# Performance work log

Measured on AMD Instinct MI355X. Metric: run time of the kernel, lower is better.

The kernel has to match this reference:

```python
import jax, jax.numpy as jnp
import numpy as np

N_NODES = 50000
N_EDGES = 320000
B = 4096          # subgraph batch: users/items/subg nodes
IN_N = 64         # in_nfeats
IN_E = 16         # in_efeats
OUT_E = 2 * IN_E  # out_edge_feats = in_efeats*2
H = 4             # num_heads
D = 64            # latent dim per layer (latent_dim=[64,64])
L = 2             # num EGAT layers


def setup_inputs() -> dict:
    key = jax.random.key(0)
    ks = iter(jax.random.split(key, 48))
    def nrm(shape, s=0.05):
        return jax.random.normal(next(ks), shape, dtype=jnp.float32) * s
    inp = {}
    inp['x'] = jax.random.normal(next(ks), (N_NODES, IN_N), dtype=jnp.float32)
    inp['efeat'] = jax.random.normal(next(ks), (N_EDGES, IN_E), dtype=jnp.float32)
    inp['efeat2'] = jax.random.normal(next(ks), (N_EDGES, IN_N), dtype=jnp.float32)
    inp['edge_mask'] = (jax.random.uniform(next(ks), (N_EDGES,)) > 0.1).astype(jnp.float32)
    inp['edge_mask2'] = (jax.random.uniform(next(ks), (N_EDGES,)) > 0.1).astype(jnp.float32)
    inp['src'] = jax.random.randint(next(ks), (N_EDGES,), 0, N_NODES, dtype=jnp.int32)
    inp['dst'] = jax.random.randint(next(ks), (N_EDGES,), 0, N_NODES, dtype=jnp.int32)
    inp['user_idx'] = jnp.arange(0, B, dtype=jnp.int32)          # ntype==0
    inp['item_idx'] = jnp.arange(B, 2 * B, dtype=jnp.int32)      # ntype==1
    inp['subg_idx'] = jnp.arange(2 * B, 3 * B, dtype=jnp.int32)  # ntype==-1
    # stacked per-layer EGAT params (layer dims identical since IN_N == D)
    inp['loc_wni'] = nrm((L, D, H * OUT_E))
    inp['loc_wnj'] = nrm((L, D, H * OUT_E))
    inp['loc_we'] = nrm((L, IN_E, H * OUT_E))
    inp['loc_attn'] = nrm((L, H, OUT_E))
    inp['loc_wnode'] = nrm((L, D, H * D))
    inp['agg1_w'] = nrm((L, H * D, D))
    inp['agg1_b'] = jnp.zeros((L, D), jnp.float32)
    inp['glob_wni'] = nrm((L, D, H * OUT_E))
    inp['glob_wnj'] = nrm((L, D, H * OUT_E))
    inp['glob_we'] = nrm((L, IN_N, H * OUT_E))
    inp['glob_attn'] = nrm((L, H, OUT_E))
    inp['glob_wnode'] = nrm((L, D, H * D))
    inp['agg2_w'] = nrm((L, H * D, D))
    inp['agg2_b'] = jnp.zeros((L, D), jnp.float32)
    inp['w1_ui'] = nrm((2 * L * D, 128))
    inp['b1_ui'] = jnp.zeros((128,), jnp.float32)
    inp['w1_sg'] = nrm((L * D, 128))
    inp['b1_sg'] = jnp.zeros((128,), jnp.float32)
    inp['w2_ui'] = nrm((128, 1))
    inp['b2_ui'] = jnp.zeros((1,), jnp.float32)
    inp['w2_sg'] = nrm((128, 1))
    inp['b2_sg'] = jnp.zeros((1,), jnp.float32)
    return inp


def _egat(x, e, norm, src, dst, wni, wnj, we, attn, wnode):
    # edge feature: f_ij = LeakyReLU(W_ni x_i + W_nj x_j + W_e e_ij), slope 0.2 (DGL EGATConv)
    f = (x @ wni)[src] + (x @ wnj)[dst] + e @ we            # (E, H*OUT_E)
    f = jax.nn.leaky_relu(f.reshape(-1, H, OUT_E), 0.2)
    scores = jnp.einsum('ehd,hd->eh', f, attn)              # (E, H)
    # edge softmax over incoming edges of each dst node
    m = jax.ops.segment_max(scores, dst, num_segments=N_NODES)
    m = jnp.where(jnp.isfinite(m), m, 0.0)
    ex = jnp.exp(scores - m[dst])
    denom = jax.ops.segment_sum(ex, dst, num_segments=N_NODES)
    a = ex / (denom[dst] + 1e-9)
    a = a * norm[:, None]                                    # per-edge norm (edge mask) weighting
    fn = (x @ wnode).reshape(-1, H, D)                       # (N, H, D)
    msg = fn[src] * a[:, :, None]                            # (E, H, D)
    out = jax.ops.segment_sum(msg, dst, num_segments=N_NODES)
    return out, a


def reference(x, efeat, efeat2, edge_mask, edge_mask2, src, dst, user_idx, item_idx, subg_idx,
              loc_wni, loc_wnj, loc_we, loc_attn, loc_wnode, agg1_w, agg1_b,
              glob_wni, glob_wnj, glob_we, glob_attn, glob_wnode, agg2_w, agg2_b,
              w1_ui, b1_ui, w1_sg, b1_sg, w2_ui, b2_ui, w2_sg, b2_sg):
    h = x
    ui_states, sg_states = [], []
    for l in range(L):
        out, _ = _egat(h, efeat, edge_mask, src, dst,
                       loc_wni[l], loc_wnj[l], loc_we[l], loc_attn[l], loc_wnode[l])
        h = jax.nn.elu(out.reshape(N_NODES, H * D) @ agg1_w[l] + agg1_b[l])
        ui_states.append(h)
        out, _ = _egat(h, efeat2, edge_mask2, src, dst,
                       glob_wni[l], glob_wnj[l], glob_we[l], glob_attn[l], glob_wnode[l])
        h = jax.nn.leaky_relu(out.reshape(N_NODES, H * D) @ agg2_w[l] + agg2_b[l], 0.01)
        sg_states.append(h)
    ui = jnp.concatenate(ui_states, axis=1)   # (N, L*D)
    sg = jnp.concatenate(sg_states, axis=1)   # (N, L*D)
    ui_x = jnp.concatenate([ui[user_idx], ui[item_idx]], axis=1)  # (B, 2*L*D)
    sg_x = sg[subg_idx]                                           # (B, L*D)
    ui_h = jax.nn.relu(ui_x @ w1_ui + b1_ui)  # dropout is identity in eval
    sg_h = jax.nn.relu(sg_x @ w1_sg + b1_sg)
    ui_out = jax.nn.sigmoid(ui_h @ w2_ui + b2_ui)[:, 0]
    sg_out = jax.nn.sigmoid(sg_h @ w2_sg + b2_sg)[:, 0]
    return (sg_out, ui_out)
```

## Files before the change

kernel.cpp:

```cpp
#include <hip/hip_runtime.h>
#include <math.h>

#define NN 50000
#define NE 320000
#define BATCH 4096

typedef __bf16 bf16x8 __attribute__((ext_vector_type(8)));
typedef float floatx4 __attribute__((ext_vector_type(4)));
typedef unsigned short ushort;
typedef unsigned int uint;

__device__ __forceinline__ float lrelu02(float x) { return x > 0.f ? x : 0.2f * x; }
__device__ __forceinline__ float b2f(ushort h) { return __uint_as_float(((uint)h) << 16); }
__device__ __forceinline__ float b2f_lo(uint u) { return __uint_as_float(u << 16); }
__device__ __forceinline__ float b2f_hi(uint u) { return __uint_as_float(u & 0xffff0000u); }
__device__ __forceinline__ ushort f2b(float x) {
    uint u = __float_as_uint(x);
    return (ushort)((u + 0x7fffu + ((u >> 16) & 1u)) >> 16);
}
__device__ __forceinline__ void unpack8(uint4 v, float* f) {
    f[0] = b2f_lo(v.x); f[1] = b2f_hi(v.x); f[2] = b2f_lo(v.y); f[3] = b2f_hi(v.y);
    f[4] = b2f_lo(v.z); f[5] = b2f_hi(v.z); f[6] = b2f_lo(v.w); f[7] = b2f_hi(v.w);
}

template <int NT, int EPI, int AF32>
__global__ __launch_bounds__(256) void gemm_bf16(
    const void* __restrict__ Av, int lda, int M, int K, int Kreal,
    const ushort* __restrict__ Bt,
    ushort* __restrict__ outb,
    const float* __restrict__ bias, int act,
    const int* __restrict__ ridx,
    const int* __restrict__ srcv, const int* __restrict__ dstv,
    const ushort* __restrict__ xfull, const float* __restrict__ attn,
    float* __restrict__ scv)
{
    constexpr int NC = 16 * NT;
    __shared__ __align__(16) ushort As[64 * 32];
    __shared__ __align__(16) ushort Bs[NC * 32];
    const int tid = threadIdx.x;
    const int row0 = blockIdx.x << 6;
    const int w = tid >> 6, lane = tid & 63;
    const int quad = lane >> 4, l16 = lane & 15;
    const int arow = tid >> 2, akc = (tid & 3) << 3;
    int agrow = -1;
    if (row0 + arow < M) agrow = ridx ? ridx[row0 + arow] : (row0 + arow);

    floatx4 acc[NT];
#pragma unroll
    for (int c = 0; c < NT; c++)
#pragma unroll
        for (int r = 0; r < 4; r++) acc[c][r] = 0.f;

    for (int kt = 0; kt < K; kt += 32) {
        uint4 av = make_uint4(0u, 0u, 0u, 0u);
        if (AF32) {
            if (agrow >= 0 && kt + akc < Kreal) {
                const float* ap = (const float*)Av + (size_t)agrow * lda + kt + akc;
                float4 f0 = *(const float4*)ap;
                float4 f1 = *(const float4*)(ap + 4);
                av.x = (uint)f2b(f0.x) | ((uint)f2b(f0.y) << 16);
                av.y = (uint)f2b(f0.z) | ((uint)f2b(f0.w) << 16);
                av.z = (uint)f2b(f1.x) | ((uint)f2b(f1.y) << 16);
                av.w = (uint)f2b(f1.z) | ((uint)f2b(f1.w) << 16);
            }
        } else {
            if (agrow >= 0)
                av = *(const uint4*)((const ushort*)Av + (size_t)agrow * lda + kt + akc);
        }
        *(uint4*)(As + arow * 32 + akc) = av;
#pragma unroll
        for (int it = 0; it < NT / 4; it++) {
            int idx = it * 256 + tid;
            int bn = idx >> 2, bkc = (idx & 3) << 3;
            *(uint4*)(Bs + bn * 32 + bkc) =
                *(const uint4*)(Bt + (size_t)bn * K + kt + bkc);
        }
        __syncthreads();
        bf16x8 af = *(const bf16x8*)(As + (16 * w + l16) * 32 + quad * 8);
#pragma unroll
        for (int c = 0; c < NT; c++) {
            bf16x8 bfv = *(const bf16x8*)(Bs + (16 * c + l16) * 32 + quad * 8);
            acc[c] = __builtin_amdgcn_mfma_f32_16x16x32_bf16(af, bfv, acc[c], 0, 0, 0);
        }
        __syncthreads();
    }

    if (EPI == 1) {
#pragma unroll
        for (int r = 0; r < 4; r++) {
            int gr = row0 + 16 * w + quad * 4 + r;
            if (gr < M) {
#pragma unroll
                for (int c = 0; c < NT; c++) {
                    int col = 16 * c + l16;
                    float v = acc[c][r] + bias[col];
                    if (act == 0) v = v > 0.f ? v : (__expf(v) - 1.f);
                    else          v = v > 0.f ? v : 0.01f * v;
                    outb[(size_t)gr * 64 + col] = f2b(v);
                }
            }
        }
    } else if (EPI == 2) {
#pragma unroll
        for (int r = 0; r < 4; r++) {
            int gr = row0 + 16 * w + quad * 4 + r;
            if (gr < M) {
                uint4 o0, o1;
                o0.x = (uint)f2b(acc[0][r])  | ((uint)f2b(acc[1][r])  << 16);
                o0.y = (uint)f2b(acc[2][r])  | ((uint)f2b(acc[3][r])  << 16);
                o0.z = (uint)f2b(acc[4][r])  | ((uint)f2b(acc[5][r])  << 16);
                o0.w = (uint)f2b(acc[6][r])  | ((uint)f2b(acc[7][r])  << 16);
                o1.x = (uint)f2b(acc[8][r])  | ((uint)f2b(acc[9][r])  << 16);
                o1.y = (uint)f2b(acc[10][r]) | ((uint)f2b(acc[11][r]) << 16);
                o1.z = (uint)f2b(acc[12][r]) | ((uint)f2b(acc[13][r]) << 16);
                o1.w = (uint)f2b(acc[14][r]) | ((uint)f2b(acc[15][r]) << 16);
                *(uint4*)(outb + (size_t)gr * 256 + l16 * 8) = o0;
                *(uint4*)(outb + (size_t)gr * 256 + 128 + l16 * 8) = o1;
            }
        }
    } else if (EPI == 3) {
        float av8[8];
#pragma unroll
        for (int c = 0; c < 8; c++)
            av8[c] = attn[(c >> 1) * 32 + (c & 1) * 16 + l16];
#pragma unroll
        for (int r = 0; r < 4; r++) {
            int gr = row0 + 16 * w + quad * 4 + r;
            if (gr < M) {
                int s = srcv[gr], d = dstv[gr];
                float xi8[8], xj8[8];
                unpack8(*(const uint4*)(xfull + (size_t)s * 256 + l16 * 8), xi8);
                unpack8(*(const uint4*)(xfull + (size_t)d * 256 + 128 + l16 * 8), xj8);
                float ph[4] = {0.f, 0.f, 0.f, 0.f};
#pragma unroll
                for (int c = 0; c < 8; c++) {
                    float f = lrelu02(acc[c][r] + xi8[c] + xj8[c]);
                    ph[c >> 1] = fmaf(f, av8[c], ph[c >> 1]);
                }
#pragma unroll
                for (int m = 1; m < 16; m <<= 1) {
#pragma unroll
                    for (int h = 0; h < 4; h++) ph[h] += __shfl_xor(ph[h], m);
                }
                if (l16 == 0)
                    *(float4*)(scv + (size_t)gr * 4) =
                        make_float4(ph[0], ph[1], ph[2], ph[3]);
            }
        }
    }
}

__global__ void k_count(const int* __restrict__ dst, int* __restrict__ deg, int E)
{
    for (int i = blockIdx.x * blockDim.x + threadIdx.x; i < E; i += gridDim.x * blockDim.x)
        atomicAdd(&deg[dst[i]], 1);
}

__global__ __launch_bounds__(256) void scan_local(
    const int* __restrict__ deg, int* __restrict__ rowptr, int* __restrict__ partials, int N)
{
    __shared__ int sd[256];
    int tid = threadIdx.x;
    int i = blockIdx.x * 256 + tid;
    int v = (i < N) ? deg[i] : 0;
    sd[tid] = v; __syncthreads();
#pragma unroll
    for (int off = 1; off < 256; off <<= 1) {
        int t = (tid >= off) ? sd[tid - off] : 0;
        __syncthreads();
        sd[tid] += t;
        __syncthreads();
    }
    if (i < N) rowptr[i] = sd[tid] - v;
    if (tid == 255) partials[blockIdx.x] = sd[255];
}

__global__ __launch_bounds__(256) void scan_partials(int* __restrict__ partials, int nb)
{
    __shared__ int sd[256];
    int tid = threadIdx.x;
    int v = (tid < nb) ? partials[tid] : 0;
    sd[tid] = v; __syncthreads();
#pragma unroll
    for (int off = 1; off < 256; off <<= 1) {
        int t = (tid >= off) ? sd[tid - off] : 0;
        __syncthreads();
        sd[tid] += t;
        __syncthreads();
    }
    if (tid < nb) partials[tid] = sd[tid] - v;
}

__global__ void scan_add(int* __restrict__ rowptr, const int* __restrict__ partials, int N, int E)
{
    int i = blockIdx.x * 256 + threadIdx.x;
    if (i < N) rowptr[i] += partials[i >> 8];
    if (i == 0) rowptr[N] = E;
}

__global__ void k_scatter_perm(const int* __restrict__ dst, const int* __restrict__ rowptr,
                               int* __restrict__ cnt, const int* __restrict__ src,
                               const float* __restrict__ m1, const float* __restrict__ m2,
                               int* __restrict__ srcp, int* __restrict__ dstp,
                               int* __restrict__ eidx,
                               float* __restrict__ m1p, float* __restrict__ m2p, int E)
{
    for (int i = blockIdx.x * blockDim.x + threadIdx.x; i < E; i += gridDim.x * blockDim.x) {
        int d = dst[i];
        int p = rowptr[d] + atomicAdd(&cnt[d], 1);
        srcp[p] = src[i];
        dstp[p] = d;
        eidx[p] = i;
        m1p[p] = m1[i];
        m2p[p] = m2[i];
    }
}

__global__ void k_cvt(const float* __restrict__ in, ushort* __restrict__ out, int n)
{
    for (int i = blockIdx.x * blockDim.x + threadIdx.x; i < n; i += gridDim.x * blockDim.x)
        out[i] = f2b(in[i]);
}

__global__ void k_prep_ninj_all(const float* __restrict__ loc_wni, const float* __restrict__ loc_wnj,
                                const float* __restrict__ glob_wni, const float* __restrict__ glob_wnj,
                                ushort* __restrict__ B)
{
    int e = blockIdx.x >> 6;
    int idx = (blockIdx.x & 63) * 256 + threadIdx.x;
    int layer = e >> 1, gl = e & 1;
    const float* wni = (gl ? glob_wni : loc_wni) + layer * 64 * 128;
    const float* wnj = (gl ? glob_wnj : loc_wnj) + layer * 64 * 128;
    int n = idx >> 6, k = idx & 63;
    float v = (n < 128) ? wni[k * 128 + n] : wnj[k * 128 + (n - 128)];
    B[e * 16384 + idx] = f2b(v);
}

__global__ void k_prep_we_all(const float* __restrict__ loc_we, const float* __restrict__ glob_we,
                              ushort* __restrict__ B)
{
    int b = blockIdx.x;
    int e, K, Kreal, idx;
    const float* we;
    if (b < 32) { int layer = b >> 4; e = layer * 2; K = 32; Kreal = 16;
                  we = loc_we + layer * 16 * 128; idx = (b & 15) * 256 + threadIdx.x; }
    else        { int layer = (b - 32) >> 5; e = layer * 2 + 1; K = 64; Kreal = 64;
                  we = glob_we + layer * 64 * 128; idx = ((b - 32) & 31) * 256 + threadIdx.x; }
    int n = idx / K, k = idx % K;
    B[e * 8192 + idx] = (k < Kreal) ? f2b(we[k * 128 + n]) : (ushort)0;
}

__global__ void k_fold_all(const float* __restrict__ loc_wnode, const float* __restrict__ agg1_w,
                           const float* __restrict__ glob_wnode, const float* __restrict__ agg2_w,
                           ushort* __restrict__ B)
{
    int e = blockIdx.x >> 6;
    int idx = (blockIdx.x & 63) * 256 + threadIdx.x;
    int layer = e >> 1, gl = e & 1;
    const float* wnode = (gl ? glob_wnode : loc_wnode) + layer * 64 * 256;
    const float* aggw  = (gl ? agg2_w : agg1_w) + layer * 256 * 64;
    int j = idx >> 8, col = idx & 255;
    int h = col >> 6, ii = col & 63;
    float s = 0.f;
#pragma unroll 8
    for (int k = 0; k < 64; k++)
        s = fmaf(wnode[ii * 256 + h * 64 + k], aggw[(h * 64 + k) * 64 + j], s);
    B[e * 16384 + j * 256 + col] = f2b(s);
}

__global__ __launch_bounds__(256) void node_fused(
    const float* __restrict__ scv,
    const int* __restrict__ rowptr, const int* __restrict__ srcp,
    const float* __restrict__ maskp,
    const ushort* __restrict__ hsrc,
    ushort* __restrict__ zb)
{
    int tid = threadIdx.x;
    int n = (blockIdx.x << 4) | (tid >> 4);
    int sl = tid & 15;
    int beg = rowptr[n], end = rowptr[n + 1];
    float l0 = 0.f, l1 = 0.f, l2 = 0.f, l3 = 0.f;
    float acc[4][4] = {};
#pragma unroll 2
    for (int i = beg; i < end; i++) {
        float4 s4 = *(const float4*)(scv + (size_t)i * 4);
        float mk = maskp[i];
        int s = srcp[i];
        uint2 hvv = *(const uint2*)(hsrc + (size_t)s * 64 + sl * 4);
        float t0 = __expf(s4.x), t1 = __expf(s4.y), t2 = __expf(s4.z), t3 = __expf(s4.w);
        l0 += t0; l1 += t1; l2 += t2; l3 += t3;
        float a0 = t0 * mk, a1 = t1 * mk, a2 = t2 * mk, a3 = t3 * mk;
        float hv[4] = { b2f_lo(hvv.x), b2f_hi(hvv.x), b2f_lo(hvv.y), b2f_hi(hvv.y) };
#pragma unroll
        for (int c = 0; c < 4; c++) {
            acc[0][c] = fmaf(a0, hv[c], acc[0][c]);
            acc[1][c] = fmaf(a1, hv[c], acc[1][c]);
            acc[2][c] = fmaf(a2, hv[c], acc[2][c]);
            acc[3][c] = fmaf(a3, hv[c], acc[3][c]);
        }
    }
    float inv[4] = { 1.f / (l0 + 1e-9f), 1.f / (l1 + 1e-9f),
                     1.f / (l2 + 1e-9f), 1.f / (l3 + 1e-9f) };
#pragma unroll
    for (int h = 0; h < 4; h++) {
        uint2 o;
        o.x = (uint)f2b(acc[h][0] * inv[h]) | ((uint)f2b(acc[h][1] * inv[h]) << 16);
        o.y = (uint)f2b(acc[h][2] * inv[h]) | ((uint)f2b(acc[h][3] * inv[h]) << 16);
        *(uint2*)(zb + (size_t)n * 256 + h * 64 + sl * 4) = o;
    }
}

__global__ __launch_bounds__(256) void final_ui(
    const ushort* __restrict__ s0, const ushort* __restrict__ s1,
    const int* __restrict__ uidx, const int* __restrict__ iidx,
    const float* __restrict__ w1, const float* __restrict__ b1,
    const float* __restrict__ w2, const float* __restrict__ b2, float* __restrict__ out)
{
    __shared__ float xs[4][256];
    int tid = threadIdx.x, wid = tid >> 6, lane = tid & 63;
    int r = (blockIdx.x << 2) + wid;
    int u = uidx[r], it = iidx[r];
    xs[wid][lane]       = b2f(s0[(size_t)u * 64 + lane]);
    xs[wid][64 + lane]  = b2f(s1[(size_t)u * 64 + lane]);
    xs[wid][128 + lane] = b2f(s0[(size_t)it * 64 + lane]);
    xs[wid][192 + lane] = b2f(s1[(size_t)it * 64 + lane]);
    __syncthreads();
    int c = lane << 1;
    float a0 = b1[c], a1 = b1[c + 1];
    for (int k = 0; k < 256; k++) {
        float xv = xs[wid][k];
        float2 wv = *(const float2*)(w1 + (size_t)k * 128 + c);
        a0 = fmaf(xv, wv.x, a0);
        a1 = fmaf(xv, wv.y, a1);
    }
    a0 = fmaxf(a0, 0.f);
    a1 = fmaxf(a1, 0.f);
    float2 w2v = *(const float2*)(w2 + c);
    float p = a0 * w2v.x + a1 * w2v.y;
#pragma unroll
    for (int mm = 1; mm < 64; mm <<= 1) p += __shfl_xor(p, mm);
    if (lane == 0) out[r] = 1.f / (1.f + __expf(-(p + b2[0])));
}

__global__ __launch_bounds__(256) void final_sg(
    const ushort* __restrict__ s0, const ushort* __restrict__ s1,
    const int* __restrict__ gidx,
    const float* __restrict__ w1, const float* __restrict__ b1,
    const float* __restrict__ w2, const float* __restrict__ b2, float* __restrict__ out)
{
    __shared__ float xs[4][128];
    int tid = threadIdx.x, wid = tid >> 6, lane = tid & 63;
    int r = (blockIdx.x << 2) + wid;
    int n = gidx[r];
    xs[wid][lane]      = b2f(s0[(size_t)n * 64 + lane]);
    xs[wid][64 + lane] = b2f(s1[(size_t)n * 64 + lane]);
    __syncthreads();
    int c = lane << 1;
    float a0 = b1[c], a1 = b1[c + 1];
    for (int k = 0; k < 128; k++) {
        float xv = xs[wid][k];
        float2 wv = *(const float2*)(w1 + (size_t)k * 128 + c);
        a0 = fmaf(xv, wv.x, a0);
        a1 = fmaf(xv, wv.y, a1);
    }
    a0 = fmaxf(a0, 0.f);
    a1 = fmaxf(a1, 0.f);
    float2 w2v = *(const float2*)(w2 + c);
    float p = a0 * w2v.x + a1 * w2v.y;
#pragma unroll
    for (int mm = 1; mm < 64; mm <<= 1) p += __shfl_xor(p, mm);
    if (lane == 0) out[r] = 1.f / (1.f + __expf(-(p + b2[0])));
}

extern "C" void kernel_launch(void* const* d_in, const int* in_sizes, int n_in,
                              void* d_out, int out_size, void* d_ws, size_t ws_size,
                              hipStream_t stream)
{
    const float* x       = (const float*)d_in[0];
    const float* efeat   = (const float*)d_in[1];
    const float* efeat2  = (const float*)d_in[2];
    const float* mask1   = (const float*)d_in[3];
    const float* mask2   = (const float*)d_in[4];
    const int*   src     = (const int*)d_in[5];
    const int*   dst     = (const int*)d_in[6];
    const int*   uidx    = (const int*)d_in[7];
    const int*   iidx    = (const int*)d_in[8];
    const int*   gidx    = (const int*)d_in[9];
    const float* loc_wni = (const float*)d_in[10];
    const float* loc_wnj = (const float*)d_in[11];
    const float* loc_we  = (const float*)d_in[12];
    const float* loc_attn= (const float*)d_in[13];
    const float* loc_wnode=(const float*)d_in[14];
    const float* agg1_w  = (const float*)d_in[15];
    const float* agg1_b  = (const float*)d_in[16];
    const float* glob_wni= (const float*)d_in[17];
    const float* glob_wnj= (const float*)d_in[18];
    const float* glob_we = (const float*)d_in[19];
    const float* glob_attn=(const float*)d_in[20];
    const float* glob_wnode=(const float*)d_in[21];
    const float* agg2_w  = (const float*)d_in[22];
    const float* agg2_b  = (const float*)d_in[23];
    const float* w1_ui   = (const float*)d_in[24];
    const float* b1_ui   = (const float*)d_in[25];
    const float* w1_sg   = (const float*)d_in[26];
    const float* b1_sg   = (const float*)d_in[27];
    const float* w2_ui   = (const float*)d_in[28];
    const float* b2_ui   = (const float*)d_in[29];
    const float* w2_sg   = (const float*)d_in[30];
    const float* b2_sg   = (const float*)d_in[31];

    char* wsp = (char*)d_ws;
    auto carve = [&](size_t bytes) { char* p = wsp; wsp += (bytes + 255) & ~(size_t)255; return p; };
    ushort* xfull = (ushort*)carve((size_t)NN * 256 * 2);
    ushort* zb    = (ushort*)carve((size_t)NN * 256 * 2);
    ushort* hb[5];
    for (int i = 0; i < 5; i++) hb[i] = (ushort*)carve((size_t)NN * 64 * 2);
    float*  scv   = (float*)carve((size_t)NE * 16);
    float*  m1p   = (float*)carve((size_t)NE * 4);
    float*  m2p   = (float*)carve((size_t)NE * 4);
    int*    srcp  = (int*)carve((size_t)NE * 4);
    int*    dstp  = (int*)carve((size_t)NE * 4);
    int*    eidx  = (int*)carve((size_t)NE * 4);
    ushort* Bninj = (ushort*)carve(4 * 16384 * 2);
    ushort* Bwe   = (ushort*)carve(4 * 8192 * 2);
    ushort* Bfold = (ushort*)carve(4 * 16384 * 2);
    int* deg      = (int*)carve(NN * 4);
    int* rowptr   = (int*)carve((NN + 4) * 4);
    int* partials = (int*)carve(256 * 4);

    k_prep_ninj_all<<<256, 256, 0, stream>>>(loc_wni, loc_wnj, glob_wni, glob_wnj, Bninj);
    k_prep_we_all<<<96, 256, 0, stream>>>(loc_we, glob_we, Bwe);
    k_fold_all<<<256, 256, 0, stream>>>(loc_wnode, agg1_w, glob_wnode, agg2_w, Bfold);
    hipMemsetAsync(deg, 0, NN * sizeof(int), stream);
    k_count<<<1280, 256, 0, stream>>>(dst, deg, NE);
    scan_local<<<196, 256, 0, stream>>>(deg, rowptr, partials, NN);
    scan_partials<<<1, 256, 0, stream>>>(partials, 196);
    scan_add<<<196, 256, 0, stream>>>(rowptr, partials, NN, NE);
    hipMemsetAsync(deg, 0, NN * sizeof(int), stream);
    k_scatter_perm<<<1280, 256, 0, stream>>>(dst, rowptr, deg, src, mask1, mask2,
                                             srcp, dstp, eidx, m1p, m2p, NE);
    k_cvt<<<3200, 256, 0, stream>>>(x, hb[0], NN * 64);

    auto egat = [&](const ushort* hin, int e, const float* maskp, const float* attn,
                    const float* aggb, int act, ushort* hout) {
        int is_glob = e & 1;
        gemm_bf16<16, 2, 0><<<782, 256, 0, stream>>>(hin, 64, NN, 64, 64,
                                                     Bninj + e * 16384, xfull,
                                                     nullptr, 0, nullptr, nullptr,
                                                     nullptr, nullptr, nullptr, nullptr);
        if (is_glob)
            gemm_bf16<8, 3, 1><<<5000, 256, 0, stream>>>(efeat2, 64, NE, 64, 64,
                                                         Bwe + e * 8192, nullptr,
                                                         nullptr, 0, eidx, srcp, dstp,
                                                         xfull, attn, scv);
        else
            gemm_bf16<8, 3, 1><<<5000, 256, 0, stream>>>(efeat, 16, NE, 32, 16,
                                                         Bwe + e * 8192, nullptr,
                                                         nullptr, 0, eidx, srcp, dstp,
                                                         xfull, attn, scv);
        node_fused<<<NN / 16, 256, 0, stream>>>(scv, rowptr, srcp, maskp, hin, zb);
        gemm_bf16<4, 1, 0><<<782, 256, 0, stream>>>(zb, 256, NN, 256, 256,
                                                    Bfold + e * 16384, hout,
                                                    aggb, act, nullptr, nullptr,
                                                    nullptr, nullptr, nullptr, nullptr);
    };

    egat(hb[0], 0, m1p, loc_attn,        agg1_b,      0, hb[1]);
    egat(hb[1], 1, m2p, glob_attn,       agg2_b,      1, hb[2]);
    egat(hb[2], 2, m1p, loc_attn + 128,  agg1_b + 64, 0, hb[3]);
    egat(hb[3], 3, m2p, glob_attn + 128, agg2_b + 64, 1, hb[4]);

    float* out = (float*)d_out;
    final_sg<<<BATCH / 4, 256, 0, stream>>>(hb[2], hb[4], gidx, w1_sg, b1_sg, w2_sg, b2_sg, out);
    final_ui<<<BATCH / 4, 256, 0, stream>>>(hb[1], hb[3], uidx, iidx, w1_ui, b1_ui, w2_ui, b2_ui, out + BATCH);
}
```

Measured before the change: 640.0 us.

## Widen GEMM K tile to 64 and prefetch edge gather before MMA loop

Adds a KTILE template parameter so each GEMM iteration stages two 32-wide K panels at once. This halves the number of barrier pairs for K=64 and K=256 GEMMs and drops the trailing sync on the last iteration. The edge-score GEMM now issues its random xfull gathers for src and dst before the main loop, so their latency overlaps the A/B loads and MFMAs. The cost is more shared memory and more registers held live during the loop, which may lower occupancy.

After: 656.6 us. 2.6% more time.

```diff
diff --git a/kernel.cpp b/kernel.cpp
--- a/kernel.cpp
+++ b/kernel.cpp
@@ -23,7 +23,7 @@
     f[4] = b2f_lo(v.z); f[5] = b2f_hi(v.z); f[6] = b2f_lo(v.w); f[7] = b2f_hi(v.w);
 }
 
-template <int NT, int EPI, int AF32>
+template <int NT, int EPI, int AF32, int KTILE>
 __global__ __launch_bounds__(256) void gemm_bf16(
     const void* __restrict__ Av, int lda, int M, int K, int Kreal,
     const ushort* __restrict__ Bt,
@@ -35,54 +35,78 @@
     float* __restrict__ scv)
 {
     constexpr int NC = 16 * NT;
-    __shared__ __align__(16) ushort As[64 * 32];
-    __shared__ __align__(16) ushort Bs[NC * 32];
+    constexpr int PAN = KTILE / 32;
+    __shared__ __align__(16) ushort As[PAN * 64 * 32];
+    __shared__ __align__(16) ushort Bs[PAN * NC * 32];
     const int tid = threadIdx.x;
     const int row0 = blockIdx.x << 6;
     const int w = tid >> 6, lane = tid & 63;
     const int quad = lane >> 4, l16 = lane & 15;
-    const int arow = tid >> 2, akc = (tid & 3) << 3;
+    const int arow = tid >> 2, asub = tid & 3;
     int agrow = -1;
     if (row0 + arow < M) agrow = ridx ? ridx[row0 + arow] : (row0 + arow);
 
+    uint4 pxi[4], pxj[4];
+    if (EPI == 3) {
+#pragma unroll
+        for (int r = 0; r < 4; r++) {
+            int gr = row0 + 16 * w + quad * 4 + r;
+            if (gr < M) {
+                int s = srcv[gr], d = dstv[gr];
+                pxi[r] = *(const uint4*)(xfull + (size_t)s * 256 + l16 * 8);
+                pxj[r] = *(const uint4*)(xfull + (size_t)d * 256 + 128 + l16 * 8);
+            }
+        }
+    }
+
     floatx4 acc[NT];
 #pragma unroll
     for (int c = 0; c < NT; c++)
 #pragma unroll
         for (int r = 0; r < 4; r++) acc[c][r] = 0.f;
 
-    for (int kt = 0; kt < K; kt += 32) {
-        uint4 av = make_uint4(0u, 0u, 0u, 0u);
-        if (AF32) {
-            if (agrow >= 0 && kt + akc < Kreal) {
-                const float* ap = (const float*)Av + (size_t)agrow * lda + kt + akc;
-                float4 f0 = *(const float4*)ap;
-                float4 f1 = *(const float4*)(ap + 4);
-                av.x = (uint)f2b(f0.x) | ((uint)f2b(f0.y) << 16);
-                av.y = (uint)f2b(f0.z) | ((uint)f2b(f0.w) << 16);
-                av.z = (uint)f2b(f1.x) | ((uint)f2b(f1.y) << 16);
-                av.w = (uint)f2b(f1.z) | ((uint)f2b(f1.w) << 16);
-            }
-        } else {
-            if (agrow >= 0)
-                av = *(const uint4*)((const ushort*)Av + (size_t)agrow * lda + kt + akc);
-        }
-        *(uint4*)(As + arow * 32 + akc) = av;
-#pragma unroll
-        for (int it = 0; it < NT / 4; it++) {
+    for (int kt = 0; kt < K; kt += KTILE) {
+#pragma unroll
+        for (int u = 0; u < PAN; u++) {
+            int colb = asub * (KTILE / 4) + u * 8;
+            uint4 av = make_uint4(0u, 0u, 0u, 0u);
+            if (AF32) {
+                if (agrow >= 0 && kt + colb < Kreal) {
+                    const float* ap = (const float*)Av + (size_t)agrow * lda + kt + colb;
+                    float4 f0 = *(const float4*)ap;
+                    float4 f1 = *(const float4*)(ap + 4);
+                    av.x = (uint)f2b(f0.x) | ((uint)f2b(f0.y) << 16);
+                    av.y = (uint)f2b(f0.z) | ((uint)f2b(f0.w) << 16);
+                    av.z = (uint)f2b(f1.x) | ((uint)f2b(f1.y) << 16);
+                    av.w = (uint)f2b(f1.z) | ((uint)f2b(f1.w) << 16);
+                }
+            } else {
+                if (agrow >= 0)
+                    av = *(const uint4*)((const ushort*)Av + (size_t)agrow * lda + kt + colb);
+            }
+            int p = colb >> 5;
+            *(uint4*)(As + p * 2048 + arow * 32 + (colb & 31)) = av;
+        }
+#pragma unroll
+        for (int it = 0; it < (NC * KTILE) / 2048; it++) {
             int idx = it * 256 + tid;
-            int bn = idx >> 2, bkc = (idx & 3) << 3;
-            *(uint4*)(Bs + bn * 32 + bkc) =
-                *(const uint4*)(Bt + (size_t)bn * K + kt + bkc);
+            int bn = idx / (KTILE / 8);
+            int bk = (idx % (KTILE / 8)) * 8;
+            int p = bk >> 5;
+            *(uint4*)(Bs + p * NC * 32 + bn * 32 + (bk & 31)) =
+                *(const uint4*)(Bt + (size_t)bn * K + kt + bk);
         }
         __syncthreads();
-        bf16x8 af = *(const bf16x8*)(As + (16 * w + l16) * 32 + quad * 8);
-#pragma unroll
-        for (int c = 0; c < NT; c++) {
-            bf16x8 bfv = *(const bf16x8*)(Bs + (16 * c + l16) * 32 + quad * 8);
-            acc[c] = __builtin_amdgcn_mfma_f32_16x16x32_bf16(af, bfv, acc[c], 0, 0, 0);
-        }
-        __syncthreads();
+#pragma unroll
+        for (int ks = 0; ks < PAN; ks++) {
+            bf16x8 af = *(const bf16x8*)(As + ks * 2048 + (16 * w + l16) * 32 + quad * 8);
+#pragma unroll
+            for (int c = 0; c < NT; c++) {
+                bf16x8 bfv = *(const bf16x8*)(Bs + ks * NC * 32 + (16 * c + l16) * 32 + quad * 8);
+                acc[c] = __builtin_amdgcn_mfma_f32_16x16x32_bf16(af, bfv, acc[c], 0, 0, 0);
+            }
+        }
+        if (kt + KTILE < K) __syncthreads();
     }
 
     if (EPI == 1) {
@@ -127,10 +151,9 @@
         for (int r = 0; r < 4; r++) {
             int gr = row0 + 16 * w + quad * 4 + r;
             if (gr < M) {
-                int s = srcv[gr], d = dstv[gr];
                 float xi8[8], xj8[8];
-                unpack8(*(const uint4*)(xfull + (size_t)s * 256 + l16 * 8), xi8);
-                unpack8(*(const uint4*)(xfull + (size_t)d * 256 + 128 + l16 * 8), xj8);
+                unpack8(pxi[r], xi8);
+                unpack8(pxj[r], xj8);
                 float ph[4] = {0.f, 0.f, 0.f, 0.f};
 #pragma unroll
                 for (int c = 0; c < 8; c++) {
@@ -444,25 +467,25 @@
     auto egat = [&](const ushort* hin, int e, const float* maskp, const float* attn,
                     const float* aggb, int act, ushort* hout) {
         int is_glob = e & 1;
-        gemm_bf16<16, 2, 0><<<782, 256, 0, stream>>>(hin, 64, NN, 64, 64,
-                                                     Bninj + e * 16384, xfull,
-                                                     nullptr, 0, nullptr, nullptr,
-                                                     nullptr, nullptr, nullptr, nullptr);
+        gemm_bf16<16, 2, 0, 64><<<782, 256, 0, stream>>>(hin, 64, NN, 64, 64,
+                                                         Bninj + e * 16384, xfull,
+                                                         nullptr, 0, nullptr, nullptr,
+                                                         nullptr, nullptr, nullptr, nullptr);
         if (is_glob)
-            gemm_bf16<8, 3, 1><<<5000, 256, 0, stream>>>(efeat2, 64, NE, 64, 64,
-                                                         Bwe + e * 8192, nullptr,
-                                                         nullptr, 0, eidx, srcp, dstp,
-                                                         xfull, attn, scv);
+            gemm_bf16<8, 3, 1, 64><<<5000, 256, 0, stream>>>(efeat2, 64, NE, 64, 64,
+                                                             Bwe + e * 8192, nullptr,
+                                                             nullptr, 0, eidx, srcp, dstp,
+                                                             xfull, attn, scv);
         else
-            gemm_bf16<8, 3, 1><<<5000, 256, 0, stream>>>(efeat, 16, NE, 32, 16,
-                                                         Bwe + e * 8192, nullptr,
-                                                         nullptr, 0, eidx, srcp, dstp,
-                                                         xfull, attn, scv);
+            gemm_bf16<8, 3, 1, 32><<<5000, 256, 0, stream>>>(efeat, 16, NE, 32, 16,
+                                                             Bwe + e * 8192, nullptr,
+                                                             nullptr, 0, eidx, srcp, dstp,
+                                                             xfull, attn, scv);
         node_fused<<<NN / 16, 256, 0, stream>>>(scv, rowptr, srcp, maskp, hin, zb);
-        gemm_bf16<4, 1, 0><<<782, 256, 0, stream>>>(zb, 256, NN, 256, 256,
-                                                    Bfold + e * 16384, hout,
-                                                    aggb, act, nullptr, nullptr,
-                                                    nullptr, nullptr, nullptr, nullptr);
+        gemm_bf16<4, 1, 0, 64><<<782, 256, 0, stream>>>(zb, 256, NN, 256, 256,
+                                                        Bfold + e * 16384, hout,
+                                                        aggb, act, nullptr, nullptr,
+                                                        nullptr, nullptr, nullptr, nullptr);
     };
 
     egat(hb[0], 0, m1p, loc_attn,        agg1_b,      0, hb[1]);
```

## Fuse node projections into edge score GEMM by concatenating K dimension

Applied to the files above, without the earlier changes.

Drops the separate per-node GEMM that wrote a 256-wide xfull buffer. The edge score kernel now gathers the raw 64-wide src and dst node features and concatenates them with the edge features along K, using a stacked weight matrix [We; Wni; Wnj] prepared once. This removes a kernel launch plus the xfull write and re-read, at the cost of more MFMA work per edge (K of 160 or 192 instead of 32 or 64) and redundant per-edge recomputation of the node projections. The GEMMs are also split into specialised kernels, and the trailing barrier after the last K step is skipped.

Result: no change. 627.9 us (-1.9%).

```diff
diff --git a/kernel.cpp b/kernel.cpp
--- a/kernel.cpp
+++ b/kernel.cpp
@@ -18,44 +18,39 @@
     uint u = __float_as_uint(x);
     return (ushort)((u + 0x7fffu + ((u >> 16) & 1u)) >> 16);
 }
-__device__ __forceinline__ void unpack8(uint4 v, float* f) {
-    f[0] = b2f_lo(v.x); f[1] = b2f_hi(v.x); f[2] = b2f_lo(v.y); f[3] = b2f_hi(v.y);
-    f[4] = b2f_lo(v.z); f[5] = b2f_hi(v.z); f[6] = b2f_lo(v.w); f[7] = b2f_hi(v.w);
-}
-
-template <int NT, int EPI, int AF32>
-__global__ __launch_bounds__(256) void gemm_bf16(
-    const void* __restrict__ Av, int lda, int M, int K, int Kreal,
+
+__global__ __launch_bounds__(256) void score_gemm(
+    const float* __restrict__ ef, int lda_ef, int ef_real, int ef_end, int KTOT,
     const ushort* __restrict__ Bt,
-    ushort* __restrict__ outb,
-    const float* __restrict__ bias, int act,
-    const int* __restrict__ ridx,
-    const int* __restrict__ srcv, const int* __restrict__ dstv,
-    const ushort* __restrict__ xfull, const float* __restrict__ attn,
-    float* __restrict__ scv)
-{
-    constexpr int NC = 16 * NT;
+    const ushort* __restrict__ hb,
+    const int* __restrict__ eidx, const int* __restrict__ srcv,
+    const int* __restrict__ dstv,
+    const float* __restrict__ attn, float* __restrict__ scv)
+{
     __shared__ __align__(16) ushort As[64 * 32];
-    __shared__ __align__(16) ushort Bs[NC * 32];
+    __shared__ __align__(16) ushort Bs[128 * 32];
     const int tid = threadIdx.x;
     const int row0 = blockIdx.x << 6;
     const int w = tid >> 6, lane = tid & 63;
     const int quad = lane >> 4, l16 = lane & 15;
-    const int arow = tid >> 2, akc = (tid & 3) << 3;
-    int agrow = -1;
-    if (row0 + arow < M) agrow = ridx ? ridx[row0 + arow] : (row0 + arow);
-
-    floatx4 acc[NT];
-#pragma unroll
-    for (int c = 0; c < NT; c++)
+    const int arow = tid >> 2, c0 = (tid & 3) << 3;
+    const int gr = row0 + arow;
+    const int e_o = eidx[gr];
+    const ushort* hs = hb + (size_t)srcv[gr] * 64;
+    const ushort* hd = hb + (size_t)dstv[gr] * 64;
+
+    floatx4 acc[8];
+#pragma unroll
+    for (int c = 0; c < 8; c++)
 #pragma unroll
         for (int r = 0; r < 4; r++) acc[c][r] = 0.f;
 
-    for (int kt = 0; kt < K; kt += 32) {
+    for (int kt = 0; kt < KTOT; kt += 32) {
         uint4 av = make_uint4(0u, 0u, 0u, 0u);
-        if (AF32) {
-            if (agrow >= 0 && kt + akc < Kreal) {
-                const float* ap = (const float*)Av + (size_t)agrow * lda + kt + akc;
+        if (kt < ef_end) {
+            int col = kt + c0;
+            if (col < ef_real) {
+                const float* ap = ef + (size_t)e_o * lda_ef + col;
                 float4 f0 = *(const float4*)ap;
                 float4 f1 = *(const float4*)(ap + 4);
                 av.x = (uint)f2b(f0.x) | ((uint)f2b(f0.y) << 16);
@@ -63,88 +58,101 @@
                 av.z = (uint)f2b(f1.x) | ((uint)f2b(f1.y) << 16);
                 av.w = (uint)f2b(f1.z) | ((uint)f2b(f1.w) << 16);
             }
+        } else if (kt < ef_end + 64) {
+            av = *(const uint4*)(hs + (kt - ef_end) + c0);
         } else {
-            if (agrow >= 0)
-                av = *(const uint4*)((const ushort*)Av + (size_t)agrow * lda + kt + akc);
-        }
-        *(uint4*)(As + arow * 32 + akc) = av;
-#pragma unroll
-        for (int it = 0; it < NT / 4; it++) {
+            av = *(const uint4*)(hd + (kt - ef_end - 64) + c0);
+        }
+        *(uint4*)(As + arow * 32 + c0) = av;
+#pragma unroll
+        for (int it = 0; it < 2; it++) {
             int idx = it * 256 + tid;
-            int bn = idx >> 2, bkc = (idx & 3) << 3;
-            *(uint4*)(Bs + bn * 32 + bkc) =
-                *(const uint4*)(Bt + (size_t)bn * K + kt + bkc);
+            int bn = idx >> 2, bk = (idx & 3) << 3;
+            *(uint4*)(Bs + bn * 32 + bk) = *(const uint4*)(Bt + (size_t)bn * KTOT + kt + bk);
         }
         __syncthreads();
         bf16x8 af = *(const bf16x8*)(As + (16 * w + l16) * 32 + quad * 8);
 #pragma unroll
-        for (int c = 0; c < NT; c++) {
+        for (int c = 0; c < 8; c++) {
             bf16x8 bfv = *(const bf16x8*)(Bs + (16 * c + l16) * 32 + quad * 8);
             acc[c] = __builtin_amdgcn_mfma_f32_16x16x32_bf16(af, bfv, acc[c], 0, 0, 0);
         }
-        __syncthreads();
-    }
-
-    if (EPI == 1) {
-#pragma unroll
-        for (int r = 0; r < 4; r++) {
-            int gr = row0 + 16 * w + quad * 4 + r;
-            if (gr < M) {
-#pragma unroll
-                for (int c = 0; c < NT; c++) {
-                    int col = 16 * c + l16;
-                    float v = acc[c][r] + bias[col];
-                    if (act == 0) v = v > 0.f ? v : (__expf(v) - 1.f);
-                    else          v = v > 0.f ? v : 0.01f * v;
-                    outb[(size_t)gr * 64 + col] = f2b(v);
-                }
-            }
-        }
-    } else if (EPI == 2) {
-#pragma unroll
-        for (int r = 0; r < 4; r++) {
-            int gr = row0 + 16 * w + quad * 4 + r;
-            if (gr < M) {
-                uint4 o0, o1;
-                o0.x = (uint)f2b(acc[0][r])  | ((uint)f2b(acc[1][r])  << 16);
-                o0.y = (uint)f2b(acc[2][r])  | ((uint)f2b(acc[3][r])  << 16);
-                o0.z = (uint)f2b(acc[4][r])  | ((uint)f2b(acc[5][r])  << 16);
-                o0.w = (uint)f2b(acc[6][r])  | ((uint)f2b(acc[7][r])  << 16);
-                o1.x = (uint)f2b(acc[8][r])  | ((uint)f2b(acc[9][r])  << 16);
-                o1.y = (uint)f2b(acc[10][r]) | ((uint)f2b(acc[11][r]) << 16);
-                o1.z = (uint)f2b(acc[12][r]) | ((uint)f2b(acc[13][r]) << 16);
-                o1.w = (uint)f2b(acc[14][r]) | ((uint)f2b(acc[15][r]) << 16);
-                *(uint4*)(outb + (size_t)gr * 256 + l16 * 8) = o0;
-                *(uint4*)(outb + (size_t)gr * 256 + 128 + l16 * 8) = o1;
-            }
-        }
-    } else if (EPI == 3) {
-        float av8[8];
-#pragma unroll
-        for (int c = 0; c < 8; c++)
-            av8[c] = attn[(c >> 1) * 32 + (c & 1) * 16 + l16];
-#pragma unroll
-        for (int r = 0; r < 4; r++) {
-            int gr = row0 + 16 * w + quad * 4 + r;
-            if (gr < M) {
-                int s = srcv[gr], d = dstv[gr];
-                float xi8[8], xj8[8];
-                unpack8(*(const uint4*)(xfull + (size_t)s * 256 + l16 * 8), xi8);
-                unpack8(*(const uint4*)(xfull + (size_t)d * 256 + 128 + l16 * 8), xj8);
-                float ph[4] = {0.f, 0.f, 0.f, 0.f};
-#pragma unroll
-                for (int c = 0; c < 8; c++) {
-                    float f = lrelu02(acc[c][r] + xi8[c] + xj8[c]);
-                    ph[c >> 1] = fmaf(f, av8[c], ph[c >> 1]);
-                }
-#pragma unroll
-                for (int m = 1; m < 16; m <<= 1) {
-#pragma unroll
-                    for (int h = 0; h < 4; h++) ph[h] += __shfl_xor(ph[h], m);
-                }
-                if (l16 == 0)
-                    *(float4*)(scv + (size_t)gr * 4) =
-                        make_float4(ph[0], ph[1], ph[2], ph[3]);
+        if (kt + 32 < KTOT) __syncthreads();
+    }
+
+    float av8[8];
+#pragma unroll
+    for (int c = 0; c < 8; c++)
+        av8[c] = attn[(c >> 1) * 32 + (c & 1) * 16 + l16];
+#pragma unroll
+    for (int r = 0; r < 4; r++) {
+        int orow = row0 + 16 * w + quad * 4 + r;
+        float ph[4] = {0.f, 0.f, 0.f, 0.f};
+#pragma unroll
+        for (int c = 0; c < 8; c++) {
+            float f = lrelu02(acc[c][r]);
+            ph[c >> 1] = fmaf(f, av8[c], ph[c >> 1]);
+        }
+#pragma unroll
+        for (int m = 1; m < 16; m <<= 1) {
+#pragma unroll
+            for (int h = 0; h < 4; h++) ph[h] += __shfl_xor(ph[h], m);
+        }
+        if (l16 == 0)
+            *(float4*)(scv + (size_t)orow * 4) = make_float4(ph[0], ph[1], ph[2], ph[3]);
+    }
+}
+
+__global__ __launch_bounds__(256) void gemm_agg(
+    const ushort* __restrict__ A, int M,
+    const ushort* __restrict__ Bt,
+    const float* __restrict__ bias, int act,
+    ushort* __restrict__ outb)
+{
+    __shared__ __align__(16) ushort As[64 * 32];
+    __shared__ __align__(16) ushort Bs[64 * 32];
+    const int tid = threadIdx.x;
+    const int row0 = blockIdx.x << 6;
+    const int w = tid >> 6, lane = tid & 63;
+    const int quad = lane >> 4, l16 = lane & 15;
+    const int arow = tid >> 2, c0 = (tid & 3) << 3;
+    const int agrow = row0 + arow;
+
+    floatx4 acc[4];
+#pragma unroll
+    for (int c = 0; c < 4; c++)
+#pragma unroll
+        for (int r = 0; r < 4; r++) acc[c][r] = 0.f;
+
+    for (int kt = 0; kt < 256; kt += 32) {
+        uint4 av = make_uint4(0u, 0u, 0u, 0u);
+        if (agrow < M)
+            av = *(const uint4*)(A + (size_t)agrow * 256 + kt + c0);
+        *(uint4*)(As + arow * 32 + c0) = av;
+        {
+            int bn = tid >> 2, bk = (tid & 3) << 3;
+            *(uint4*)(Bs + bn * 32 + bk) = *(const uint4*)(Bt + (size_t)bn * 256 + kt + bk);
+        }
+        __syncthreads();
+        bf16x8 af = *(const bf16x8*)(As + (16 * w + l16) * 32 + quad * 8);
+#pragma unroll
+        for (int c = 0; c < 4; c++) {
+            bf16x8 bfv = *(const bf16x8*)(Bs + (16 * c + l16) * 32 + quad * 8);
+            acc[c] = __builtin_amdgcn_mfma_f32_16x16x32_bf16(af, bfv, acc[c], 0, 0, 0);
+        }
+        if (kt + 32 < 256) __syncthreads();
+    }
+#pragma unroll
+    for (int r = 0; r < 4; r++) {
+        int gr = row0 + 16 * w + quad * 4 + r;
+        if (gr < M) {
+#pragma unroll
+            for (int c = 0; c < 4; c++) {
+                int col = 16 * c + l16;
+                float v = acc[c][r] + bias[col];
+                if (act == 0) v = v > 0.f ? v : (__expf(v) - 1.f);
+                else          v = v > 0.f ? v : 0.01f * v;
+                outb[(size_t)gr * 64 + col] = f2b(v);
             }
         }
     }
@@ -222,32 +230,28 @@
         out[i] = f2b(in[i]);
 }
 
-__global__ void k_prep_ninj_all(const float* __restrict__ loc_wni, const float* __restrict__ loc_wnj,
-                                const float* __restrict__ glob_wni, const float* __restrict__ glob_wnj,
-                                ushort* __restrict__ B)
-{
-    int e = blockIdx.x >> 6;
-    int idx = (blockIdx.x & 63) * 256 + threadIdx.x;
+__global__ void k_prep_score_all(const float* __restrict__ loc_we, const float* __restrict__ glob_we,
+                                 const float* __restrict__ loc_wni, const float* __restrict__ glob_wni,
+                                 const float* __restrict__ loc_wnj, const float* __restrict__ glob_wnj,
+                                 ushort* __restrict__ B)
+{
+    int idx = blockIdx.x * 256 + threadIdx.x;
+    if (idx >= 4 * 24576) return;
+    int e = idx / 24576, rem = idx % 24576;
     int layer = e >> 1, gl = e & 1;
+    int KTOT = gl ? 192 : 160;
+    int ef_end = gl ? 64 : 32;
+    int ef_real = gl ? 64 : 16;
+    if (rem >= 128 * KTOT) return;
+    int n = rem / KTOT, k = rem % KTOT;
+    const float* we  = (gl ? glob_we  + layer * 64 * 128 : loc_we  + layer * 16 * 128);
     const float* wni = (gl ? glob_wni : loc_wni) + layer * 64 * 128;
     const float* wnj = (gl ? glob_wnj : loc_wnj) + layer * 64 * 128;
-    int n = idx >> 6, k = idx & 63;
-    float v = (n < 128) ? wni[k * 128 + n] : wnj[k * 128 + (n - 128)];
-    B[e * 16384 + idx] = f2b(v);
-}
-
-__global__ void k_prep_we_all(const float* __restrict__ loc_we, const float* __restrict__ glob_we,
-                              ushort* __restrict__ B)
-{
-    int b = blockIdx.x;
-    int e, K, Kreal, idx;
-    const float* we;
-    if (b < 32) { int layer = b >> 4; e = layer * 2; K = 32; Kreal = 16;
-                  we = loc_we + layer * 16 * 128; idx = (b & 15) * 256 + threadIdx.x; }
-    else        { int layer = (b - 32) >> 5; e = layer * 2 + 1; K = 64; Kreal = 64;
-                  we = glob_we + layer * 64 * 128; idx = ((b - 32) & 31) * 256 + threadIdx.x; }
-    int n = idx / K, k = idx % K;
-    B[e * 8192 + idx] = (k < Kreal) ? f2b(we[k * 128 + n]) : (ushort)0;
+    float v;
+    if (k < ef_end)            v = (k < ef_real) ? we[k * 128 + n] : 0.f;
+    else if (k < ef_end + 64)  v = wni[(k - ef_end) * 128 + n];
+    else                       v = wnj[(k - ef_end - 64) * 128 + n];
+    B[e * 24576 + rem] = f2b(v);
 }
 
 __global__ void k_fold_all(const float* __restrict__ loc_wnode, const float* __restrict__ agg1_w,
@@ -411,7 +415,6 @@
 
     char* wsp = (char*)d_ws;
     auto carve = [&](size_t bytes) { char* p = wsp; wsp += (bytes + 255) & ~(size_t)255; return p; };
-    ushort* xfull = (ushort*)carve((size_t)NN * 256 * 2);
     ushort* zb    = (ushort*)carve((size_t)NN * 256 * 2);
     ushort* hb[5];
     for (int i = 0; i < 5; i++) hb[i] = (ushort*)carve((size_t)NN * 64 * 2);
@@ -421,15 +424,14 @@
     int*    srcp  = (int*)carve((size_t)NE * 4);
     int*    dstp  = (int*)carve((size_t)NE * 4);
     int*    eidx  = (int*)carve((size_t)NE * 4);
-    ushort* Bninj = (ushort*)carve(4 * 16384 * 2);
-    ushort* Bwe   = (ushort*)carve(4 * 8192 * 2);
+    ushort* Bsc   = (ushort*)carve(4 * 24576 * 2);
     ushort* Bfold = (ushort*)carve(4 * 16384 * 2);
     int* deg      = (int*)carve(NN * 4);
     int* rowptr   = (int*)carve((NN + 4) * 4);
     int* partials = (int*)carve(256 * 4);
 
-    k_prep_ninj_all<<<256, 256, 0, stream>>>(loc_wni, loc_wnj, glob_wni, glob_wnj, Bninj);
-    k_prep_we_all<<<96, 256, 0, stream>>>(loc_we, glob_we, Bwe);
+    k_prep_score_all<<<384, 256, 0, stream>>>(loc_we, glob_we, loc_wni, glob_wni,
+                                              loc_wnj, glob_wnj, Bsc);
     k_fold_all<<<256, 256, 0, stream>>>(loc_wnode, agg1_w, glob_wnode, agg2_w, Bfold);
     hipMemsetAsync(deg, 0, NN * sizeof(int), stream);
     k_count<<<1280, 256, 0, stream>>>(dst, deg, NE);
@@ -444,25 +446,16 @@
     auto egat = [&](const ushort* hin, int e, const float* maskp, const float* attn,
                     const float* aggb, int act, ushort* hout) {
         int is_glob = e & 1;
-        gemm_bf16<16, 2, 0><<<782, 256, 0, stream>>>(hin, 64, NN, 64, 64,
-                                                     Bninj + e * 16384, xfull,
-                                                     nullptr, 0, nullptr, nullptr,
-                                                     nullptr, nullptr, nullptr, nullptr);
         if (is_glob)
-            gemm_bf16<8, 3, 1><<<5000, 256, 0, stream>>>(efeat2, 64, NE, 64, 64,
-                                                         Bwe + e * 8192, nullptr,
-                                                         nullptr, 0, eidx, srcp, dstp,
-                                                         xfull, attn, scv);
+            score_gemm<<<5000, 256, 0, stream>>>(efeat2, 64, 64, 64, 192,
+                                                 Bsc + e * 24576, hin,
+                                                 eidx, srcp, dstp, attn, scv);
         else
-            gemm_bf16<8, 3, 1><<<5000, 256, 0, stream>>>(efeat, 16, NE, 32, 16,
-                                                         Bwe + e * 8192, nullptr,
-                                                         nullptr, 0, eidx, srcp, dstp,
-                                                         xfull, attn, scv);
+            score_gemm<<<5000, 256, 0, stream>>>(efeat, 16, 16, 32, 160,
+                                                 Bsc + e * 24576, hin,
+                                                 eidx, srcp, dstp, attn, scv);
         node_fused<<<NN / 16, 256, 0, stream>>>(scv, rowptr, srcp, maskp, hin, zb);
-        gemm_bf16<4, 1, 0><<<782, 256, 0, stream>>>(zb, 256, NN, 256, 256,
-                                                    Bfold + e * 16384, hout,
-                                                    aggb, act, nullptr, nullptr,
-                                                    nullptr, nullptr, nullptr, nullptr);
+        gemm_agg<<<782, 256, 0, stream>>>(zb, NN, Bfold + e * 16384, aggb, act, hout);
     };
 
     egat(hb[0], 0, m1p, loc_attn,        agg1_b,      0, hb[1]);
```
